# Kernel tuning notes

Measured on AMD Instinct MI355X. Metric: run time of the kernel, lower is better.

Reference implementation:

```python
import jax, jax.numpy as jnp
import numpy as np

N, E, IN_DIM, H, HEADS, L, NCLS, NTYPES, NGRAPH = 50000, 800000, 128, 128, 4, 3, 10, 8, 64
C = H // HEADS

def setup_inputs() -> dict:
    key = jax.random.key(0)
    ks = jax.random.split(key, 24)
    inp = {
        'x': jax.random.normal(ks[0], (N, IN_DIM), jnp.float32),
        'edge_index': jax.random.randint(ks[1], (2, E), 0, N, jnp.int64),
        'node_types': jax.random.randint(ks[2], (N,), 0, NTYPES, jnp.int64),
        'batch': jnp.sort(jax.random.randint(ks[3], (N,), 0, NGRAPH, jnp.int64)),
        'W_node': jax.random.normal(ks[4], (IN_DIM, H), jnp.float32) / np.sqrt(IN_DIM),
        'b_node': jnp.zeros((H,), jnp.float32),
        'type_emb': jax.random.normal(ks[5], (NTYPES, H), jnp.float32) * 0.02,
        'W_gat': jax.random.normal(ks[6], (L, H, H), jnp.float32) / np.sqrt(H),
        'a_src': jax.random.normal(ks[7], (L, HEADS, C), jnp.float32) / np.sqrt(C),
        'a_dst': jax.random.normal(ks[8], (L, HEADS, C), jnp.float32) / np.sqrt(C),
        'b_gat': jnp.zeros((L, H), jnp.float32),
        'ln_g': jnp.ones((L, H), jnp.float32),
        'ln_b': jnp.zeros((L, H), jnp.float32),
        'W1': jax.random.normal(ks[9], (H, 2 * H), jnp.float32) / np.sqrt(H),
        'b1': jnp.zeros((2 * H,), jnp.float32),
        'W2': jax.random.normal(ks[10], (2 * H, H), jnp.float32) / np.sqrt(2 * H),
        'b2': jnp.zeros((H,), jnp.float32),
        'W3': jax.random.normal(ks[11], (H, NCLS), jnp.float32) / np.sqrt(H),
        'b3': jnp.zeros((NCLS,), jnp.float32),
    }
    return inp


def _gat_layer(h, src, dst, W, asrc, adst, b):
    # h: [N,H] -> xh: [N,heads,C]
    xh = (h @ W).reshape(N, HEADS, C)
    s_src = jnp.sum(xh * asrc, axis=-1)  # [N,heads]
    s_dst = jnp.sum(xh * adst, axis=-1)
    e = jax.nn.leaky_relu(s_src[src] + s_dst[dst], 0.2)  # [E',heads]
    m = jax.ops.segment_max(e, dst, num_segments=N)      # segment softmax over dst
    ee = jnp.exp(e - m[dst])
    z = jax.ops.segment_sum(ee, dst, num_segments=N)
    alpha = ee / (z[dst] + 1e-16)
    msg = xh[src] * alpha[:, :, None]                    # [E',heads,C]
    out = jax.ops.segment_sum(msg, dst, num_segments=N)
    return out.reshape(N, H) + b


def _layernorm(x, g, b, eps=1e-5):
    mu = jnp.mean(x, -1, keepdims=True)
    var = jnp.mean((x - mu) ** 2, -1, keepdims=True)
    return (x - mu) * jax.lax.rsqrt(var + eps) * g + b


def reference(x, edge_index, node_types, batch, W_node, b_node, type_emb,
              W_gat, a_src, a_dst, b_gat, ln_g, ln_b, W1, b1, W2, b2, W3, b3):
    # PyG GATConv adds self-loops by default
    loops = jnp.arange(N, dtype=edge_index.dtype)
    src = jnp.concatenate([edge_index[0], loops])
    dst = jnp.concatenate([edge_index[1], loops])

    h = x @ W_node + b_node + type_emb[node_types]
    for l in range(L):
        h_prev = h
        h = _gat_layer(h, src, dst, W_gat[l], a_src[l], a_dst[l], b_gat[l])
        h = _layernorm(h, ln_g[l], ln_b[l])
        h = jax.nn.relu(h + h_prev)

    # global_mean_pool over batch (the global-attention h_graph is dead code: overwritten)
    sums = jax.ops.segment_sum(h, batch, num_segments=NGRAPH)
    cnt = jax.ops.segment_sum(jnp.ones((N,), h.dtype), batch, num_segments=NGRAPH)
    hg = sums / jnp.maximum(cnt, 1.0)[:, None]

    z = jax.nn.relu(hg @ W1 + b1)
    z = jax.nn.relu(z @ W2 + b2)
    return z @ W3 + b3
```

## Files before the change

### kernel.cpp

```cpp
#include <hip/hip_runtime.h>
#include <hip/hip_bf16.h>

#define NN 50000
#define EE 800000
#define IN_DIM 128
#define HH 128
#define HEADS 4
#define CC 32
#define LL 3
#define NCLS 10
#define NGRAPH 64
#define SNB ((NN + 1023) / 1024)

using short8 = __attribute__((ext_vector_type(8))) short;
using f32x4 = __attribute__((ext_vector_type(4))) float;

__device__ inline float lrelu(float x) { return fmaxf(x, 0.2f * x); }
__device__ inline float fexp(float x) { return __expf(x); }

__device__ inline float bf2f(ushort u) {
    union { uint32_t i; float f; } c;
    c.i = ((uint32_t)u) << 16;
    return c.f;
}
__device__ inline ushort f2bf(float f) {
    union { float f; uint32_t i; } c;
    c.f = f;
    uint32_t x = c.i;
    uint32_t r = (x + 0x7fffu + ((x >> 16) & 1u)) >> 16;
    return (ushort)r;
}

__device__ inline float wred_sum(float v) {
#pragma unroll
    for (int m = 32; m >= 1; m >>= 1) v += __shfl_xor(v, m, 64);
    return v;
}

__device__ inline float pick4(int h, float a, float b, float c, float d) {
    float ab = (h & 1) ? b : a;
    float cd = (h & 1) ? d : c;
    return (h & 2) ? cd : ab;
}

__global__ __launch_bounds__(256) void convert_x(const float* __restrict__ x,
                                                 ushort* __restrict__ xb) {
    int u = blockIdx.x * 256 + threadIdx.x;
    const float4* x4 = (const float4*)x;
    float4 f0 = x4[u * 2];
    float4 f1 = x4[u * 2 + 1];
    short8 o;
    o[0] = (short)f2bf(f0.x); o[1] = (short)f2bf(f0.y);
    o[2] = (short)f2bf(f0.z); o[3] = (short)f2bf(f0.w);
    o[4] = (short)f2bf(f1.x); o[5] = (short)f2bf(f1.y);
    o[6] = (short)f2bf(f1.z); o[7] = (short)f2bf(f1.w);
    ((short8*)xb)[u] = o;
}

__global__ __launch_bounds__(256) void prep_weights(const float* __restrict__ W_node,
                                                    const float* __restrict__ W_gat,
                                                    ushort* __restrict__ WT) {
    int b = blockIdx.x;
    const float* W = (b == 0) ? W_node : (W_gat + (size_t)(b - 1) * 16384);
    ushort* D = WT + (size_t)b * 16384;
    int t = threadIdx.x;
    int n = t >> 1;
    int k0 = (t & 1) * 64;
    for (int kk = 0; kk < 64; kk++) {
        int k = k0 + kk;
        float v = W[k * 128 + n];
        int u = (k >> 3) ^ (n & 7);
        D[n * 128 + u * 8 + (k & 7)] = f2bf(v);
    }
}

template <int MODE>
__global__ __launch_bounds__(256) void gemm_mfma(
    const ushort* __restrict__ Abf, const ushort* __restrict__ WT,
    ushort* __restrict__ out_bf,
    const float* __restrict__ bias, const int* __restrict__ ntypes,
    const float* __restrict__ temb, int nrows) {
    __shared__ ushort wlds[16384];
    int tid = threadIdx.x;
    int lane = tid & 63;
    int wid = tid >> 6;

    {
        const short8* src = (const short8*)WT;
        short8* dst = (short8*)wlds;
#pragma unroll
        for (int i = 0; i < 8; i++) dst[i * 256 + tid] = src[i * 256 + tid];
    }

    int rbase = blockIdx.x * 64 + wid * 16;
    int arow = rbase + (lane & 15);
    if (arow >= nrows) arow = nrows - 1;
    const short8* arow_p = (const short8*)(Abf + (size_t)arow * 128);
    short8 afr[4];
#pragma unroll
    for (int ks = 0; ks < 4; ks++) afr[ks] = arow_p[ks * 4 + (lane >> 4)];

    __syncthreads();

    f32x4 acc[8];
#pragma unroll
    for (int i = 0; i < 8; i++) acc[i] = (f32x4){0.f, 0.f, 0.f, 0.f};

    int cgrp = lane & 15;
    int kgrp = lane >> 4;
#pragma unroll
    for (int ks = 0; ks < 4; ks++) {
        short8 a = afr[ks];
#pragma unroll
        for (int nt = 0; nt < 8; nt++) {
            int n = nt * 16 + cgrp;
            int u = (ks * 4 + kgrp) ^ (n & 7);
            short8 b = *(const short8*)&wlds[n * 128 + u * 8];
            acc[nt] = __builtin_amdgcn_mfma_f32_16x16x32_bf16(a, b, acc[nt], 0, 0, 0);
        }
    }

    int nts[4];
    if (MODE == 1) {
#pragma unroll
        for (int r = 0; r < 4; r++) {
            int row = rbase + kgrp * 4 + r;
            nts[r] = (row < nrows) ? ntypes[row] : 0;
        }
    }
#pragma unroll
    for (int nt = 0; nt < 8; nt++) {
        int colc = nt * 16 + cgrp;
#pragma unroll
        for (int r = 0; r < 4; r++) {
            int row = rbase + kgrp * 4 + r;
            if (row < nrows) {
                float v = acc[nt][r];
                if (MODE == 1) v += bias[colc] + temb[nts[r] * 128 + colc];
                out_bf[(size_t)row * 128 + colc] = f2bf(v);
            }
        }
    }
}

__global__ __launch_bounds__(256) void attn_scores(
    const ushort* __restrict__ xh, const float* __restrict__ asrc,
    const float* __restrict__ adst, float* __restrict__ s_src,
    float* __restrict__ s_dst, int n) {
    int tid = threadIdx.x;
    int node = blockIdx.x * 16 + (tid >> 4);
    int g = tid & 15;
    if (node >= n) return;
    short8 xv = *(const short8*)(xh + (size_t)node * 128 + g * 8);
    const float4* as4 = (const float4*)(asrc + g * 8);
    const float4* ad4 = (const float4*)(adst + g * 8);
    float4 a0 = as4[0], a1 = as4[1];
    float4 d0 = ad4[0], d1 = ad4[1];
    float xf[8];
#pragma unroll
    for (int k = 0; k < 8; k++) xf[k] = bf2f((ushort)xv[k]);
    float ps = xf[0] * a0.x + xf[1] * a0.y + xf[2] * a0.z + xf[3] * a0.w +
               xf[4] * a1.x + xf[5] * a1.y + xf[6] * a1.z + xf[7] * a1.w;
    float pd = xf[0] * d0.x + xf[1] * d0.y + xf[2] * d0.z + xf[3] * d0.w +
               xf[4] * d1.x + xf[5] * d1.y + xf[6] * d1.z + xf[7] * d1.w;
    ps += __shfl_xor(ps, 1, 64); ps += __shfl_xor(ps, 2, 64);
    pd += __shfl_xor(pd, 1, 64); pd += __shfl_xor(pd, 2, 64);
    if ((g & 3) == 0) {
        s_src[node * 4 + (g >> 2)] = ps;
        s_dst[node * 4 + (g >> 2)] = pd;
    }
}

__global__ void count_edges(const int* __restrict__ dst, int* __restrict__ deg, int ne) {
    int i = blockIdx.x * blockDim.x + threadIdx.x;
    if (i < ne) atomicAdd(&deg[dst[i]], 1);
}

__global__ __launch_bounds__(1024) void scan_local(const int* __restrict__ cnt,
                                                   int* __restrict__ rp,
                                                   int* __restrict__ btot, int n) {
    __shared__ int lds[1024];
    int t = threadIdx.x;
    int i = blockIdx.x * 1024 + t;
    int v = (i < n) ? cnt[i] : 0;
    lds[t] = v;
    __syncthreads();
    for (int off = 1; off < 1024; off <<= 1) {
        int u = (t >= off) ? lds[t - off] : 0;
        __syncthreads();
        lds[t] += u;
        __syncthreads();
    }
    if (i < n) rp[i] = lds[t] - v;
    if (t == 1023) btot[blockIdx.x] = lds[1023];
}

__global__ __launch_bounds__(64) void scan_btot(int* __restrict__ btot) {
    int t = threadIdx.x;
    int v = (t < SNB) ? btot[t] : 0;
#pragma unroll
    for (int off = 1; off < 64; off <<= 1) {
        int u = __shfl_up(v, off, 64);
        if (t >= off) v += u;
    }
    if (t < SNB) btot[t] = v;
}

__global__ __launch_bounds__(1024) void scan_add(int* __restrict__ rp,
                                                 const int* __restrict__ btot, int n) {
    int b = blockIdx.x;
    int i = b * 1024 + threadIdx.x;
    int add = (b == 0) ? 0 : btot[b - 1];
    if (i < n) rp[i] += add;
    if (i == 0) rp[n] = EE;
}

__global__ void fill_edges(const int* __restrict__ ei, const int* __restrict__ row_ptr,
                           int* __restrict__ fill, int* __restrict__ col, int ne) {
    int i = blockIdx.x * blockDim.x + threadIdx.x;
    if (i < ne) {
        int d = ei[ne + i];
        int pos = row_ptr[d] + atomicAdd(&fill[d], 1);
        col[pos] = ei[i];
    }
}

__global__ __launch_bounds__(256) void gat_aggregate(
    const ushort* __restrict__ xh, const float* __restrict__ ssrc,
    const float* __restrict__ sdst, const int* __restrict__ row_ptr,
    const int* __restrict__ col, const float* __restrict__ bg,
    const float* __restrict__ lng, const float* __restrict__ lnb,
    ushort* __restrict__ h, int n) {
    int wid = threadIdx.x >> 6;
    int lane = threadIdx.x & 63;
    int node = blockIdx.x * 4 + wid;
    if (node >= n) return;

    int base = row_ptr[node];
    int deg = row_ptr[node + 1] - base;

    float4 sd = ((const float4*)sdst)[node];
    float4 ssf = ((const float4*)ssrc)[node];

    int eg = lane >> 4;
    int g = lane & 15;
    int head = g >> 2;
    float sdH = pick4(head, sd.x, sd.y, sd.z, sd.w);
    float esH = lrelu(pick4(head, ssf.x, ssf.y, ssf.z, ssf.w) + sdH);

    float acc[8];
#pragma unroll
    for (int k = 0; k < 8; k++) acc[k] = 0.f;
    float z = 0.f;

    if (eg == 0) {
        float w = fexp(esH);
        z = w;
        short8 xv = *(const short8*)(xh + (size_t)node * 128 + g * 8);
#pragma unroll
        for (int k = 0; k < 8; k++) acc[k] += w * bf2f((ushort)xv[k]);
    }

    int nit = (deg + 3) >> 2;
#pragma unroll 2
    for (int t = 0; t < nit; t++) {
        int j = t * 4 + eg;
        if (j < deg) {
            int s = col[base + j];
            float4 ss = ((const float4*)ssrc)[s];
            float sH = pick4(head, ss.x, ss.y, ss.z, ss.w);
            float w = fexp(lrelu(sH + sdH));
            z += w;
            short8 xv = *(const short8*)(xh + (size_t)s * 128 + g * 8);
#pragma unroll
            for (int k = 0; k < 8; k++) acc[k] += w * bf2f((ushort)xv[k]);
        }
    }
#pragma unroll
    for (int k = 0; k < 8; k++) {
        acc[k] += __shfl_xor(acc[k], 16, 64);
        acc[k] += __shfl_xor(acc[k], 32, 64);
    }
    z += __shfl_xor(z, 16, 64);
    z += __shfl_xor(z, 32, 64);
    float iz = 1.f / (z + 1e-16f);

    const float4* bg4 = (const float4*)(bg + g * 8);
    float4 b0 = bg4[0], b1 = bg4[1];
    float o[8];
    o[0] = acc[0] * iz + b0.x; o[1] = acc[1] * iz + b0.y;
    o[2] = acc[2] * iz + b0.z; o[3] = acc[3] * iz + b0.w;
    o[4] = acc[4] * iz + b1.x; o[5] = acc[5] * iz + b1.y;
    o[6] = acc[6] * iz + b1.z; o[7] = acc[7] * iz + b1.w;

    float ls = 0.f;
#pragma unroll
    for (int k = 0; k < 8; k++) ls += o[k];
    float mu = wred_sum(ls) * (1.f / 512.f);
    float vs = 0.f;
#pragma unroll
    for (int k = 0; k < 8; k++) {
        o[k] -= mu;
        vs += o[k] * o[k];
    }
    float var = wred_sum(vs) * (1.f / 512.f);
    float rs = rsqrtf(var + 1e-5f);

    if (eg == 0) {
        const float4* lg4 = (const float4*)(lng + g * 8);
        const float4* lb4 = (const float4*)(lnb + g * 8);
        float4 g0 = lg4[0], g1 = lg4[1];
        float4 q0 = lb4[0], q1 = lb4[1];
        ushort* hr = h + (size_t)node * 128 + g * 8;
        short8 prev = *(const short8*)hr;
        float y[8];
        y[0] = fmaxf(o[0] * rs * g0.x + q0.x + bf2f((ushort)prev[0]), 0.f);
        y[1] = fmaxf(o[1] * rs * g0.y + q0.y + bf2f((ushort)prev[1]), 0.f);
        y[2] = fmaxf(o[2] * rs * g0.z + q0.z + bf2f((ushort)prev[2]), 0.f);
        y[3] = fmaxf(o[3] * rs * g0.w + q0.w + bf2f((ushort)prev[3]), 0.f);
        y[4] = fmaxf(o[4] * rs * g1.x + q1.x + bf2f((ushort)prev[4]), 0.f);
        y[5] = fmaxf(o[5] * rs * g1.y + q1.y + bf2f((ushort)prev[5]), 0.f);
        y[6] = fmaxf(o[6] * rs * g1.z + q1.z + bf2f((ushort)prev[6]), 0.f);
        y[7] = fmaxf(o[7] * rs * g1.w + q1.w + bf2f((ushort)prev[7]), 0.f);
        short8 ob;
#pragma unroll
        for (int k = 0; k < 8; k++) ob[k] = (short)f2bf(y[k]);
        *(short8*)hr = ob;
    }
}

__global__ __launch_bounds__(256) void pool_kernel(const ushort* __restrict__ h,
                                                   const int* __restrict__ batch,
                                                   float* __restrict__ sums,
                                                   int* __restrict__ cnts, int n) {
    int c = threadIdx.x & 127;
    int half = threadIdx.x >> 7;
    int n0 = blockIdx.x * 64;
    float acc = 0.f;
    int cur = -1;
    for (int idx = half; idx < 64; idx += 2) {
        int node = n0 + idx;
        if (node >= n) break;
        int g = batch[node];
        if (g != cur) {
            if (cur >= 0) atomicAdd(&sums[cur * 128 + c], acc);
            cur = g;
            acc = 0.f;
        }
        acc += bf2f(h[(size_t)node * 128 + c]);
    }
    if (cur >= 0) atomicAdd(&sums[cur * 128 + c], acc);

    if (c == 0) {
        int cnt = 0, curg = -1;
        for (int idx = half; idx < 64; idx += 2) {
            int node = n0 + idx;
            if (node >= n) break;
            int g = batch[node];
            if (g != curg) {
                if (curg >= 0) atomicAdd(&cnts[curg], cnt);
                curg = g;
                cnt = 0;
            }
            cnt++;
        }
        if (curg >= 0) atomicAdd(&cnts[curg], cnt);
    }
}

__global__ __launch_bounds__(256) void head_kernel(
    const float* __restrict__ sums, const int* __restrict__ cnts,
    const float* __restrict__ W1, const float* __restrict__ b1,
    const float* __restrict__ W2, const float* __restrict__ b2,
    const float* __restrict__ W3, const float* __restrict__ b3,
    float* __restrict__ out) {
    __shared__ float hg[128], z1[256], z2[128];
    int g = blockIdx.x;
    int t = threadIdx.x;
    if (t < 128) hg[t] = sums[g * 128 + t] / fmaxf((float)cnts[g], 1.f);
    __syncthreads();
    {
        float acc = b1[t];
        for (int k = 0; k < 128; k++) acc += hg[k] * W1[k * 256 + t];
        z1[t] = fmaxf(acc, 0.f);
    }
    __syncthreads();
    if (t < 128) {
        float acc = b2[t];
        for (int k = 0; k < 256; k++) acc += z1[k] * W2[k * 128 + t];
        z2[t] = fmaxf(acc, 0.f);
    }
    __syncthreads();
    if (t < NCLS) {
        float acc = b3[t];
        for (int k = 0; k < 128; k++) acc += z2[k] * W3[k * NCLS + t];
        out[g * NCLS + t] = acc;
    }
}

extern "C" void kernel_launch(void* const* d_in, const int* in_sizes, int n_in,
                              void* d_out, int out_size, void* d_ws, size_t ws_size,
                              hipStream_t stream) {
    const float* x = (const float*)d_in[0];
    const int* ei = (const int*)d_in[1];
    const int* ntypes = (const int*)d_in[2];
    const int* batch = (const int*)d_in[3];
    const float* W_node = (const float*)d_in[4];
    const float* b_node = (const float*)d_in[5];
    const float* temb = (const float*)d_in[6];
    const float* W_gat = (const float*)d_in[7];
    const float* a_src = (const float*)d_in[8];
    const float* a_dst = (const float*)d_in[9];
    const float* b_gat = (const float*)d_in[10];
    const float* ln_g = (const float*)d_in[11];
    const float* ln_b = (const float*)d_in[12];
    const float* W1 = (const float*)d_in[13];
    const float* b1 = (const float*)d_in[14];
    const float* W2 = (const float*)d_in[15];
    const float* b2 = (const float*)d_in[16];
    const float* W3 = (const float*)d_in[17];
    const float* b3 = (const float*)d_in[18];
    float* out = (float*)d_out;

    char* ws = (char*)d_ws;
    size_t off = 0;
    auto alloc = [&](size_t bytes) {
        void* p = ws + off;
        off += (bytes + 255) & ~(size_t)255;
        return p;
    };
    ushort* hb = (ushort*)alloc((size_t)NN * 128 * 2);
    ushort* xhb = (ushort*)alloc((size_t)NN * 128 * 2);
    ushort* WT = (ushort*)alloc((size_t)4 * 16384 * 2);
    float* ssrc = (float*)alloc((size_t)NN * 4 * 4);
    float* sdst = (float*)alloc((size_t)NN * 4 * 4);
    int* rowp = (int*)alloc((size_t)(NN + 1) * 4);
    int* fillc = (int*)alloc((size_t)NN * 4);
    int* col = (int*)alloc((size_t)EE * 4);
    float* psum = (float*)alloc((size_t)NGRAPH * 128 * 4);
    int* pcnt = (int*)alloc((size_t)NGRAPH * 4);
    int* btot = (int*)alloc((size_t)SNB * 4);

    hipError_t e0;
    e0 = hipMemsetAsync(fillc, 0, (size_t)NN * 4, stream); (void)e0;
    e0 = hipMemsetAsync(psum, 0, (size_t)NGRAPH * 128 * 4, stream); (void)e0;
    e0 = hipMemsetAsync(pcnt, 0, (size_t)NGRAPH * 4, stream); (void)e0;

    convert_x<<<3125, 256, 0, stream>>>(x, xhb);
    prep_weights<<<4, 256, 0, stream>>>(W_node, W_gat, WT);

    count_edges<<<(EE + 255) / 256, 256, 0, stream>>>(ei + EE, fillc, EE);
    scan_local<<<SNB, 1024, 0, stream>>>(fillc, rowp, btot, NN);
    scan_btot<<<1, 64, 0, stream>>>(btot);
    scan_add<<<SNB, 1024, 0, stream>>>(rowp, btot, NN);
    e0 = hipMemsetAsync(fillc, 0, (size_t)NN * 4, stream); (void)e0;
    fill_edges<<<(EE + 255) / 256, 256, 0, stream>>>(ei, rowp, fillc, col, EE);

    int gemm_grid = (NN + 63) / 64;
    gemm_mfma<1><<<gemm_grid, 256, 0, stream>>>(xhb, WT, hb, b_node, ntypes, temb, NN);

    for (int l = 0; l < LL; l++) {
        gemm_mfma<0><<<gemm_grid, 256, 0, stream>>>(hb, WT + (size_t)(l + 1) * 16384, xhb,
                                                    nullptr, nullptr, nullptr, NN);
        attn_scores<<<(NN + 15) / 16, 256, 0, stream>>>(xhb, a_src + l * HEADS * CC,
                                                        a_dst + l * HEADS * CC, ssrc, sdst, NN);
        gat_aggregate<<<(NN + 3) / 4, 256, 0, stream>>>(
            xhb, ssrc, sdst, rowp, col, b_gat + l * 128, ln_g + l * 128, ln_b + l * 128,
            hb, NN);
    }

    pool_kernel<<<(NN + 63) / 64, 256, 0, stream>>>(hb, batch, psum, pcnt, NN);
    head_kernel<<<NGRAPH, 256, 0, stream>>>(psum, pcnt, W1, b1, W2, b2, W3, b3, out);
}
```

Baseline: 366.1 us.

## Record per-edge CSR slots and process 8 edges in parallel per wave in aggregation

The edge-count pass now stores each edge's atomic return value as its slot, so the fill pass writes col without a second round of atomics and without re-zeroing the counters. The GAT aggregation kernel now splits each wave into 8 edge groups of 8 lanes, each lane owning 16 channels, instead of 4 groups of 16 lanes with 8 channels each. This doubles the number of neighbour gathers in flight per wave, at the cost of more accumulator registers and one more shuffle-reduction step. The slot approach also needs an extra 3.2 MB edge buffer.

```diff
diff --git a/kernel.cpp b/kernel.cpp
--- a/kernel.cpp
+++ b/kernel.cpp
@@ -171,9 +171,10 @@
     }
 }
 
-__global__ void count_edges(const int* __restrict__ dst, int* __restrict__ deg, int ne) {
+__global__ void count_slot(const int* __restrict__ dst, int* __restrict__ deg,
+                           int* __restrict__ slot, int ne) {
     int i = blockIdx.x * blockDim.x + threadIdx.x;
-    if (i < ne) atomicAdd(&deg[dst[i]], 1);
+    if (i < ne) slot[i] = atomicAdd(&deg[dst[i]], 1);
 }
 
 __global__ __launch_bounds__(1024) void scan_local(const int* __restrict__ cnt,
@@ -215,13 +216,12 @@
     if (i == 0) rp[n] = EE;
 }
 
-__global__ void fill_edges(const int* __restrict__ ei, const int* __restrict__ row_ptr,
-                           int* __restrict__ fill, int* __restrict__ col, int ne) {
+__global__ void fill_pass(const int* __restrict__ ei, const int* __restrict__ row_ptr,
+                          const int* __restrict__ slot, int* __restrict__ col, int ne) {
     int i = blockIdx.x * blockDim.x + threadIdx.x;
     if (i < ne) {
         int d = ei[ne + i];
-        int pos = row_ptr[d] + atomicAdd(&fill[d], 1);
-        col[pos] = ei[i];
+        col[row_ptr[d] + slot[i]] = ei[i];
     }
 }
 
@@ -242,90 +242,114 @@
     float4 sd = ((const float4*)sdst)[node];
     float4 ssf = ((const float4*)ssrc)[node];
 
-    int eg = lane >> 4;
-    int g = lane & 15;
-    int head = g >> 2;
+    int eg = lane >> 3;
+    int g = lane & 7;
+    int head = g >> 1;
     float sdH = pick4(head, sd.x, sd.y, sd.z, sd.w);
     float esH = lrelu(pick4(head, ssf.x, ssf.y, ssf.z, ssf.w) + sdH);
 
-    float acc[8];
-#pragma unroll
-    for (int k = 0; k < 8; k++) acc[k] = 0.f;
+    float acc[16];
+#pragma unroll
+    for (int k = 0; k < 16; k++) acc[k] = 0.f;
     float z = 0.f;
 
     if (eg == 0) {
         float w = fexp(esH);
         z = w;
-        short8 xv = *(const short8*)(xh + (size_t)node * 128 + g * 8);
-#pragma unroll
-        for (int k = 0; k < 8; k++) acc[k] += w * bf2f((ushort)xv[k]);
-    }
-
-    int nit = (deg + 3) >> 2;
+        const short8* xr = (const short8*)(xh + (size_t)node * 128 + g * 16);
+        short8 x0 = xr[0], x1 = xr[1];
+#pragma unroll
+        for (int k = 0; k < 8; k++) {
+            acc[k] += w * bf2f((ushort)x0[k]);
+            acc[k + 8] += w * bf2f((ushort)x1[k]);
+        }
+    }
+
+    int nit = (deg + 7) >> 3;
 #pragma unroll 2
     for (int t = 0; t < nit; t++) {
-        int j = t * 4 + eg;
+        int j = t * 8 + eg;
         if (j < deg) {
             int s = col[base + j];
             float4 ss = ((const float4*)ssrc)[s];
             float sH = pick4(head, ss.x, ss.y, ss.z, ss.w);
             float w = fexp(lrelu(sH + sdH));
             z += w;
-            short8 xv = *(const short8*)(xh + (size_t)s * 128 + g * 8);
-#pragma unroll
-            for (int k = 0; k < 8; k++) acc[k] += w * bf2f((ushort)xv[k]);
-        }
-    }
-#pragma unroll
-    for (int k = 0; k < 8; k++) {
+            const short8* xr = (const short8*)(xh + (size_t)s * 128 + g * 16);
+            short8 x0 = xr[0], x1 = xr[1];
+#pragma unroll
+            for (int k = 0; k < 8; k++) {
+                acc[k] += w * bf2f((ushort)x0[k]);
+                acc[k + 8] += w * bf2f((ushort)x1[k]);
+            }
+        }
+    }
+#pragma unroll
+    for (int k = 0; k < 16; k++) {
+        acc[k] += __shfl_xor(acc[k], 8, 64);
         acc[k] += __shfl_xor(acc[k], 16, 64);
         acc[k] += __shfl_xor(acc[k], 32, 64);
     }
+    z += __shfl_xor(z, 8, 64);
     z += __shfl_xor(z, 16, 64);
     z += __shfl_xor(z, 32, 64);
     float iz = 1.f / (z + 1e-16f);
 
-    const float4* bg4 = (const float4*)(bg + g * 8);
-    float4 b0 = bg4[0], b1 = bg4[1];
-    float o[8];
-    o[0] = acc[0] * iz + b0.x; o[1] = acc[1] * iz + b0.y;
-    o[2] = acc[2] * iz + b0.z; o[3] = acc[3] * iz + b0.w;
-    o[4] = acc[4] * iz + b1.x; o[5] = acc[5] * iz + b1.y;
-    o[6] = acc[6] * iz + b1.z; o[7] = acc[7] * iz + b1.w;
+    const float4* bg4 = (const float4*)(bg + g * 16);
+    float o[16];
+#pragma unroll
+    for (int q = 0; q < 4; q++) {
+        float4 b = bg4[q];
+        o[q * 4 + 0] = acc[q * 4 + 0] * iz + b.x;
+        o[q * 4 + 1] = acc[q * 4 + 1] * iz + b.y;
+        o[q * 4 + 2] = acc[q * 4 + 2] * iz + b.z;
+        o[q * 4 + 3] = acc[q * 4 + 3] * iz + b.w;
+    }
 
     float ls = 0.f;
 #pragma unroll
-    for (int k = 0; k < 8; k++) ls += o[k];
-    float mu = wred_sum(ls) * (1.f / 512.f);
+    for (int k = 0; k < 16; k++) ls += o[k];
+    float mu = wred_sum(ls) * (1.f / 1024.f);
     float vs = 0.f;
 #pragma unroll
-    for (int k = 0; k < 8; k++) {
+    for (int k = 0; k < 16; k++) {
         o[k] -= mu;
         vs += o[k] * o[k];
     }
-    float var = wred_sum(vs) * (1.f / 512.f);
+    float var = wred_sum(vs) * (1.f / 1024.f);
     float rs = rsqrtf(var + 1e-5f);
 
     if (eg == 0) {
-        const float4* lg4 = (const float4*)(lng + g * 8);
-        const float4* lb4 = (const float4*)(lnb + g * 8);
-        float4 g0 = lg4[0], g1 = lg4[1];
-        float4 q0 = lb4[0], q1 = lb4[1];
-        ushort* hr = h + (size_t)node * 128 + g * 8;
-        short8 prev = *(const short8*)hr;
-        float y[8];
-        y[0] = fmaxf(o[0] * rs * g0.x + q0.x + bf2f((ushort)prev[0]), 0.f);
-        y[1] = fmaxf(o[1] * rs * g0.y + q0.y + bf2f((ushort)prev[1]), 0.f);
-        y[2] = fmaxf(o[2] * rs * g0.z + q0.z + bf2f((ushort)prev[2]), 0.f);
-        y[3] = fmaxf(o[3] * rs * g0.w + q0.w + bf2f((ushort)prev[3]), 0.f);
-        y[4] = fmaxf(o[4] * rs * g1.x + q1.x + bf2f((ushort)prev[4]), 0.f);
-        y[5] = fmaxf(o[5] * rs * g1.y + q1.y + bf2f((ushort)prev[5]), 0.f);
-        y[6] = fmaxf(o[6] * rs * g1.z + q1.z + bf2f((ushort)prev[6]), 0.f);
-        y[7] = fmaxf(o[7] * rs * g1.w + q1.w + bf2f((ushort)prev[7]), 0.f);
-        short8 ob;
-#pragma unroll
-        for (int k = 0; k < 8; k++) ob[k] = (short)f2bf(y[k]);
-        *(short8*)hr = ob;
+        const float4* lg4 = (const float4*)(lng + g * 16);
+        const float4* lb4 = (const float4*)(lnb + g * 16);
+        ushort* hr = h + (size_t)node * 128 + g * 16;
+        short8 prev0 = ((const short8*)hr)[0];
+        short8 prev1 = ((const short8*)hr)[1];
+        short8 ob0, ob1;
+#pragma unroll
+        for (int q = 0; q < 2; q++) {
+            float4 gg = lg4[q];
+            float4 qq = lb4[q];
+            float y0 = fmaxf(o[q * 4 + 0] * rs * gg.x + qq.x + bf2f((ushort)prev0[q * 4 + 0]), 0.f);
+            float y1 = fmaxf(o[q * 4 + 1] * rs * gg.y + qq.y + bf2f((ushort)prev0[q * 4 + 1]), 0.f);
+            float y2 = fmaxf(o[q * 4 + 2] * rs * gg.z + qq.z + bf2f((ushort)prev0[q * 4 + 2]), 0.f);
+            float y3 = fmaxf(o[q * 4 + 3] * rs * gg.w + qq.w + bf2f((ushort)prev0[q * 4 + 3]), 0.f);
+            ob0[q * 4 + 0] = (short)f2bf(y0); ob0[q * 4 + 1] = (short)f2bf(y1);
+            ob0[q * 4 + 2] = (short)f2bf(y2); ob0[q * 4 + 3] = (short)f2bf(y3);
+        }
+#pragma unroll
+        for (int q = 0; q < 2; q++) {
+            float4 gg = lg4[q + 2];
+            float4 qq = lb4[q + 2];
+            float y0 = fmaxf(o[8 + q * 4 + 0] * rs * gg.x + qq.x + bf2f((ushort)prev1[q * 4 + 0]), 0.f);
+            float y1 = fmaxf(o[8 + q * 4 + 1] * rs * gg.y + qq.y + bf2f((ushort)prev1[q * 4 + 1]), 0.f);
+            float y2 = fmaxf(o[8 + q * 4 + 2] * rs * gg.z + qq.z + bf2f((ushort)prev1[q * 4 + 2]), 0.f);
+            float y3 = fmaxf(o[8 + q * 4 + 3] * rs * gg.w + qq.w + bf2f((ushort)prev1[q * 4 + 3]), 0.f);
+            ob1[q * 4 + 0] = (short)f2bf(y0); ob1[q * 4 + 1] = (short)f2bf(y1);
+            ob1[q * 4 + 2] = (short)f2bf(y2); ob1[q * 4 + 3] = (short)f2bf(y3);
+        }
+        ((short8*)hr)[0] = ob0;
+        ((short8*)hr)[1] = ob1;
     }
 }
 
@@ -437,6 +461,7 @@
     int* rowp = (int*)alloc((size_t)(NN + 1) * 4);
     int* fillc = (int*)alloc((size_t)NN * 4);
     int* col = (int*)alloc((size_t)EE * 4);
+    int* slot = (int*)alloc((size_t)EE * 4);
     float* psum = (float*)alloc((size_t)NGRAPH * 128 * 4);
     int* pcnt = (int*)alloc((size_t)NGRAPH * 4);
     int* btot = (int*)alloc((size_t)SNB * 4);
@@ -449,12 +474,11 @@
     convert_x<<<3125, 256, 0, stream>>>(x, xhb);
     prep_weights<<<4, 256, 0, stream>>>(W_node, W_gat, WT);
 
-    count_edges<<<(EE + 255) / 256, 256, 0, stream>>>(ei + EE, fillc, EE);
+    count_slot<<<(EE + 255) / 256, 256, 0, stream>>>(ei + EE, fillc, slot, EE);
     scan_local<<<SNB, 1024, 0, stream>>>(fillc, rowp, btot, NN);
     scan_btot<<<1, 64, 0, stream>>>(btot);
     scan_add<<<SNB, 1024, 0, stream>>>(rowp, btot, NN);
-    e0 = hipMemsetAsync(fillc, 0, (size_t)NN * 4, stream); (void)e0;
-    fill_edges<<<(EE + 255) / 256, 256, 0, stream>>>(ei, rowp, fillc, col, EE);
+    fill_pass<<<(EE + 255) / 256, 256, 0, stream>>>(ei, rowp, slot, col, EE);
 
     int gemm_grid = (NN + 63) / 64;
     gemm_mfma<1><<<gemm_grid, 256, 0, stream>>>(xhb, WT, hb, b_node, ntypes, temb, NN);
```

Measured after the change: 347.1 us. 5.2% less time.
